# Kernel tuning notes

Measured on AMD Instinct MI355X. Metric: run time of the kernel, lower is better.

The kernel has to match this reference:

```python
import jax, jax.numpy as jnp
import numpy as np


def _pairwise_sqdist(x, y):
    # x: [B,N,D], y: [B,M,D] -> P: [B,N,M] squared euclidean distances
    xx = jnp.sum(x * x, axis=-1)            # [B,N]
    yy = jnp.sum(y * y, axis=-1)            # [B,M]
    zz = jnp.einsum('bnd,bmd->bnm', x, y)   # [B,N,M]
    return xx[:, :, None] + yy[:, None, :] - 2.0 * zz


def setup_inputs() -> dict:
    key = jax.random.key(0)
    k1, k2 = jax.random.split(key)
    B, N, M, D = 8, 4096, 4096, 256
    gts = jax.random.normal(k1, (B, N, D), dtype=jnp.float32)
    preds = jax.random.normal(k2, (B, M, D), dtype=jnp.float32)
    return {"gts": gts, "preds": preds}


def reference(gts, preds):
    P = _pairwise_sqdist(gts, preds)        # [B,N,M]
    loss_1 = jnp.sum(jnp.min(P, axis=1))    # min over gts dim (axis=1)
    loss_2 = jnp.sum(jnp.min(P, axis=2))    # min over preds dim (axis=2)
    return loss_1 + loss_2
```

## Files before the change

kernel.cpp:

```cpp
#include <hip/hip_runtime.h>

typedef int   i32x8 __attribute__((ext_vector_type(8)));
typedef float f32x4 __attribute__((ext_vector_type(4)));

#define B_   8
#define N_   4096
#define D_   256


__device__ __forceinline__ void gl_lds16(const void* g, void* l) {
  __builtin_amdgcn_global_load_lds(
      (const __attribute__((address_space(1))) unsigned int*)g,
      (__attribute__((address_space(3))) unsigned int*)l, 16, 0, 0);
}

__device__ __forceinline__ float sq8(unsigned w) {
  float f0 = __builtin_amdgcn_cvt_f32_fp8(w, 0);
  float f1 = __builtin_amdgcn_cvt_f32_fp8(w, 1);
  float f2 = __builtin_amdgcn_cvt_f32_fp8(w, 2);
  float f3 = __builtin_amdgcn_cvt_f32_fp8(w, 3);
  return f0 * f0 + f1 * f1 + f2 * f2 + f3 * f3;
}

__global__ __launch_bounds__(256) void prep_kernel(
    const float* __restrict__ x, const float* __restrict__ y,
    unsigned char* __restrict__ Xf, unsigned char* __restrict__ Yf,
    float* __restrict__ xx, float* __restrict__ yy,
    unsigned* __restrict__ rowmin, unsigned* __restrict__ colmin,
    float* __restrict__ out)
{
  __shared__ unsigned char T[4][16 * 272];
  if (blockIdx.x == 0 && threadIdx.x == 0) out[0] = 0.f;

  const int wv = threadIdx.x >> 6, lane = threadIdx.x & 63;
  const int wid = (blockIdx.x << 2) + wv;

  const float* src; unsigned char* dst; float* nrm; unsigned* mn; int g;
  if (wid < 2048) { g = wid;        src = x; dst = Xf; nrm = xx; mn = rowmin; }
  else            { g = wid - 2048; src = y; dst = Yf; nrm = yy; mn = colmin; }

  unsigned char* tw = T[wv];
  const float* rp = src + (size_t)g * 16 * D_;
#pragma unroll
  for (int r = 0; r < 16; ++r) {
    float4 v = *(const float4*)(rp + r * D_ + lane * 4);
    unsigned u = __builtin_amdgcn_cvt_pk_fp8_f32(v.x, v.y, 0, 0);
    u = __builtin_amdgcn_cvt_pk_fp8_f32(v.z, v.w, u, 1);
    *(unsigned*)(tw + r * 272 + lane * 4) = u;
  }
  asm volatile("s_waitcnt lgkmcnt(0)" ::: "memory");
  __builtin_amdgcn_wave_barrier();

  float s = 0.f;
  const int row = lane & 15, ko = (lane >> 4) * 32;
#pragma unroll
  for (int kt = 0; kt < 2; ++kt)
#pragma unroll
    for (int h = 0; h < 2; ++h) {
      uint4 c = *(const uint4*)(tw + row * 272 + kt * 128 + ko + h * 16);
      s += sq8(c.x) + sq8(c.y) + sq8(c.z) + sq8(c.w);
      *(uint4*)(dst + ((((size_t)g * 2 + kt) * 2 + h) << 10) + lane * 16) = c;
    }
  s += __shfl_xor(s, 16, 64);
  s += __shfl_xor(s, 32, 64);
  if      (lane < 16) nrm[g * 16 + lane] = s;
  else if (lane < 32) mn[g * 16 + lane - 16] = 0x7f800000u;
}

__global__ __launch_bounds__(256, 4) void chamfer_gemm(
    const unsigned char* __restrict__ Xf, const unsigned char* __restrict__ Yf,
    const float* __restrict__ xx, const float* __restrict__ yy,
    unsigned* __restrict__ rowmin, unsigned* __restrict__ colmin)
{
  __shared__ __align__(16) unsigned char S[4][8192];
  __shared__ unsigned cmin_s[1024];

  const int bid = blockIdx.x;
  const int b   = bid & 7;
  const int rt  = (bid >> 3) & 31;
  const int cq  = bid >> 8;
  const int n0  = rt * 128;
  const int m0  = cq * 1024;

  const int t = threadIdx.x, lane = t & 63, wave = t >> 6;
  const int quad = lane >> 4, lcol = lane & 15;

#pragma unroll
  for (int i = 0; i < 4; ++i) cmin_s[t + i * 256] = 0x7f800000u;

  i32x8 af[2][2];
#pragma unroll
  for (int i = 0; i < 2; ++i) {
    const size_t g = (size_t)(b * 256 + rt * 8 + wave * 2 + i);
#pragma unroll
    for (int kt = 0; kt < 2; ++kt) {
      const uint4* p = (const uint4*)(Xf + ((g * 2 + kt) << 11));
      uint4* h = (uint4*)&af[i][kt];
      h[0] = p[lane];
      h[1] = p[64 + lane];
    }
  }

  float xv[2][4], rmin[2][4];
  const float* xxp = xx + b * N_ + n0 + wave * 32;
#pragma unroll
  for (int i = 0; i < 2; ++i)
#pragma unroll
    for (int r = 0; r < 4; ++r) {
      xv[i][r] = xxp[i * 16 + quad * 4 + r];
      rmin[i][r] = 1e30f;
    }

  const unsigned char* Ybase = Yf + ((size_t)(b * 256 + cq * 64) << 12);
  const float* yyp = yy + b * N_ + m0;

#define STAGE_B(ct_, buf_)                                                    \
  {                                                                           \
    const unsigned char* Ysrc = Ybase + ((size_t)(ct_) << 13);     \
    _Pragma("unroll")                                                         \
    for (int h2 = 0; h2 < 2; ++h2) {                                          \
      int s  = t + h2 * 256;                                                  \
      int cd = s >> 6, ln = s & 63;                                           \
      int kt = cd >> 2, hh = (cd >> 1) & 1, jj = cd & 1;                      \
      gl_lds16(Ysrc + jj * 4096 + kt * 2048 + hh * 1024 + ln * 16,            \
               (buf_) + s * 16);                                              \
    }                                                                         \
  }

  auto do_ct = [&](int ct, const unsigned char* curb) {
    float yv0 = yyp[ct * 32 + lcol];
    float yv1 = yyp[ct * 32 + 16 + lcol];

    i32x8 bq[2][2];
#pragma unroll
    for (int j = 0; j < 2; ++j)
#pragma unroll
      for (int kt = 0; kt < 2; ++kt) {
        uint4* h = (uint4*)&bq[j][kt];
        h[0] = *(const uint4*)(curb + (kt * 4 + 0 + j) * 1024 + lane * 16);
        h[1] = *(const uint4*)(curb + (kt * 4 + 2 + j) * 1024 + lane * 16);
      }

    f32x4 acc[2][2] = {};
    __builtin_amdgcn_s_setprio(1);
#pragma unroll
    for (int kt = 0; kt < 2; ++kt)
#pragma unroll
      for (int i = 0; i < 2; ++i)
#pragma unroll
        for (int j = 0; j < 2; ++j)
          acc[i][j] = __builtin_amdgcn_mfma_scale_f32_16x16x128_f8f6f4(
              af[i][kt], bq[j][kt], acc[i][j],
              0, 0,
              0, 127,
              0, 127);
    __builtin_amdgcn_s_setprio(0);

#pragma unroll
    for (int j = 0; j < 2; ++j) {
      float yv = j ? yv1 : yv0;
      float cm = 1e30f;
#pragma unroll
      for (int i = 0; i < 2; ++i)
#pragma unroll
        for (int r = 0; r < 4; ++r) {
          float a = acc[i][j][r];
          rmin[i][r] = fminf(rmin[i][r], __builtin_fmaf(-2.0f, a, yv));
          cm         = fminf(cm,         __builtin_fmaf(-2.0f, a, xv[i][r]));
        }
      atomicMin(&cmin_s[ct * 32 + j * 16 + lcol], __float_as_uint(cm + yv));
    }
  };

  STAGE_B(0, S[0]);
  STAGE_B(1, S[1]);

  for (int g = 0; g < 16; ++g) {
    __syncthreads();
    const int cur = (g & 1) * 2;
    if (g + 1 < 16) {
      const int nxt = ((g + 1) & 1) * 2;
      STAGE_B(2 * g + 2, S[nxt]);
      STAGE_B(2 * g + 3, S[nxt + 1]);
    }
    do_ct(2 * g,     S[cur]);
    do_ct(2 * g + 1, S[cur + 1]);
  }

#pragma unroll
  for (int i = 0; i < 2; ++i)
#pragma unroll
    for (int r = 0; r < 4; ++r) {
      float v = xv[i][r] + rmin[i][r];
#pragma unroll
      for (int m = 1; m < 16; m <<= 1) v = fminf(v, __shfl_xor(v, m, 64));
      if (lcol == 0)
        atomicMin(rowmin + b * N_ + n0 + wave * 32 + i * 16 + quad * 4 + r,
                  __float_as_uint(v));
    }

  __syncthreads();
#pragma unroll
  for (int i = 0; i < 4; ++i) {
    int idx = t + i * 256;
    atomicMin(colmin + b * N_ + m0 + idx, cmin_s[idx]);
  }
#undef STAGE_B
}

__global__ __launch_bounds__(256) void reduce_kernel(
    const unsigned* __restrict__ mins,
    float* __restrict__ out)
{
  int idx = blockIdx.x * 256 + threadIdx.x;
  uint4 u = ((const uint4*)mins)[idx];
  float s = __uint_as_float(u.x) + __uint_as_float(u.y)
          + __uint_as_float(u.z) + __uint_as_float(u.w);
#pragma unroll
  for (int m = 1; m < 64; m <<= 1) s += __shfl_xor(s, m, 64);
  if ((threadIdx.x & 63) == 0) atomicAdd(out, s);
}

extern "C" void kernel_launch(void* const* d_in, const int* in_sizes, int n_in,
                              void* d_out, int out_size, void* d_ws, size_t ws_size,
                              hipStream_t stream) {
  const float* gts   = (const float*)d_in[0];
  const float* preds = (const float*)d_in[1];

  char* ws = (char*)d_ws;
  const size_t XB_BYTES = (size_t)B_ * N_ * D_;
  unsigned char* Xf     = (unsigned char*)ws;
  unsigned char* Yf     = (unsigned char*)(ws + XB_BYTES);
  float*    xx     = (float*)(ws + 2 * XB_BYTES);
  float*    yy     = (float*)(ws + 2 * XB_BYTES + (size_t)B_ * N_ * 4);
  unsigned* rowmin = (unsigned*)(ws + 2 * XB_BYTES + (size_t)B_ * N_ * 8);
  unsigned* colmin = (unsigned*)(ws + 2 * XB_BYTES + (size_t)B_ * N_ * 12);

  prep_kernel<<<1024, 256, 0, stream>>>(gts, preds, Xf, Yf, xx, yy, rowmin, colmin,
                                        (float*)d_out);

  chamfer_gemm<<<1024, 256, 0, stream>>>(Xf, Yf, xx, yy, rowmin, colmin);

  reduce_kernel<<<64, 256, 0, stream>>>(rowmin, (float*)d_out);
}
```

Measured before the change: 135.5 us.

## Halve per-block column span, double grid and target 8 blocks per CU

Each chamfer_gemm block now covers 512 prediction columns instead of 1024, so the grid doubles to 2048 blocks. Per-block LDS shrinks and each column tile is 16 wide instead of 32, with the B staging reduced to one 16-byte load per thread. Launch bounds ask for 8 blocks per CU to raise occupancy and improve load balance. In exchange, each block reuses its A fragments over less work, makes more global colmin atomics, and has less MFMA work per staged tile to hide latency. The in-kernel loop still runs 16 iterations of two column tiles, which matches the halved span.

```diff
diff --git a/kernel.cpp b/kernel.cpp
--- a/kernel.cpp
+++ b/kernel.cpp
@@ -67,26 +67,26 @@
   else if (lane < 32) mn[g * 16 + lane - 16] = 0x7f800000u;
 }
 
-__global__ __launch_bounds__(256, 4) void chamfer_gemm(
+__global__ __launch_bounds__(256, 8) void chamfer_gemm(
     const unsigned char* __restrict__ Xf, const unsigned char* __restrict__ Yf,
     const float* __restrict__ xx, const float* __restrict__ yy,
     unsigned* __restrict__ rowmin, unsigned* __restrict__ colmin)
 {
-  __shared__ __align__(16) unsigned char S[4][8192];
-  __shared__ unsigned cmin_s[1024];
+  __shared__ __align__(16) unsigned char S[4][4096];
+  __shared__ unsigned cmin_s[512];
 
   const int bid = blockIdx.x;
   const int b   = bid & 7;
   const int rt  = (bid >> 3) & 31;
   const int cq  = bid >> 8;
   const int n0  = rt * 128;
-  const int m0  = cq * 1024;
+  const int m0  = cq * 512;
 
   const int t = threadIdx.x, lane = t & 63, wave = t >> 6;
   const int quad = lane >> 4, lcol = lane & 15;
 
-#pragma unroll
-  for (int i = 0; i < 4; ++i) cmin_s[t + i * 256] = 0x7f800000u;
+  cmin_s[t]       = 0x7f800000u;
+  cmin_s[t + 256] = 0x7f800000u;
 
   i32x8 af[2][2];
 #pragma unroll
@@ -111,65 +111,46 @@
       rmin[i][r] = 1e30f;
     }
 
-  const unsigned char* Ybase = Yf + ((size_t)(b * 256 + cq * 64) << 12);
+  const unsigned char* Ybase = Yf + ((size_t)(b * 256 + cq * 32) << 12);
   const float* yyp = yy + b * N_ + m0;
 
 #define STAGE_B(ct_, buf_)                                                    \
-  {                                                                           \
-    const unsigned char* Ysrc = Ybase + ((size_t)(ct_) << 13);     \
-    _Pragma("unroll")                                                         \
-    for (int h2 = 0; h2 < 2; ++h2) {                                          \
-      int s  = t + h2 * 256;                                                  \
-      int cd = s >> 6, ln = s & 63;                                           \
-      int kt = cd >> 2, hh = (cd >> 1) & 1, jj = cd & 1;                      \
-      gl_lds16(Ysrc + jj * 4096 + kt * 2048 + hh * 1024 + ln * 16,            \
-               (buf_) + s * 16);                                              \
-    }                                                                         \
-  }
+  gl_lds16(Ybase + (((size_t)(ct_)) << 12) + t * 16, (buf_) + t * 16);
 
   auto do_ct = [&](int ct, const unsigned char* curb) {
-    float yv0 = yyp[ct * 32 + lcol];
-    float yv1 = yyp[ct * 32 + 16 + lcol];
-
-    i32x8 bq[2][2];
-#pragma unroll
-    for (int j = 0; j < 2; ++j)
-#pragma unroll
-      for (int kt = 0; kt < 2; ++kt) {
-        uint4* h = (uint4*)&bq[j][kt];
-        h[0] = *(const uint4*)(curb + (kt * 4 + 0 + j) * 1024 + lane * 16);
-        h[1] = *(const uint4*)(curb + (kt * 4 + 2 + j) * 1024 + lane * 16);
+    float yv = yyp[ct * 16 + lcol];
+
+    f32x4 acc[2] = {};
+#pragma unroll
+    for (int kt = 0; kt < 2; ++kt) {
+      i32x8 bq;
+      uint4* h = (uint4*)&bq;
+      h[0] = *(const uint4*)(curb + kt * 2048 + lane * 16);
+      h[1] = *(const uint4*)(curb + kt * 2048 + 1024 + lane * 16);
+      __builtin_amdgcn_s_setprio(1);
+#pragma unroll
+      for (int i = 0; i < 2; ++i)
+        acc[i] = __builtin_amdgcn_mfma_scale_f32_16x16x128_f8f6f4(
+            af[i][kt], bq, acc[i],
+            0, 0,
+            0, 127,
+            0, 127);
+      __builtin_amdgcn_s_setprio(0);
+    }
+
+    float tc[8];
+#pragma unroll
+    for (int i = 0; i < 2; ++i)
+#pragma unroll
+      for (int r = 0; r < 4; ++r) {
+        float a = acc[i][r];
+        rmin[i][r] = fminf(rmin[i][r], __builtin_fmaf(-2.0f, a, yv));
+        tc[i * 4 + r] = __builtin_fmaf(-2.0f, a, xv[i][r]);
       }
-
-    f32x4 acc[2][2] = {};
-    __builtin_amdgcn_s_setprio(1);
-#pragma unroll
-    for (int kt = 0; kt < 2; ++kt)
-#pragma unroll
-      for (int i = 0; i < 2; ++i)
-#pragma unroll
-        for (int j = 0; j < 2; ++j)
-          acc[i][j] = __builtin_amdgcn_mfma_scale_f32_16x16x128_f8f6f4(
-              af[i][kt], bq[j][kt], acc[i][j],
-              0, 0,
-              0, 127,
-              0, 127);
-    __builtin_amdgcn_s_setprio(0);
-
-#pragma unroll
-    for (int j = 0; j < 2; ++j) {
-      float yv = j ? yv1 : yv0;
-      float cm = 1e30f;
-#pragma unroll
-      for (int i = 0; i < 2; ++i)
-#pragma unroll
-        for (int r = 0; r < 4; ++r) {
-          float a = acc[i][j][r];
-          rmin[i][r] = fminf(rmin[i][r], __builtin_fmaf(-2.0f, a, yv));
-          cm         = fminf(cm,         __builtin_fmaf(-2.0f, a, xv[i][r]));
-        }
-      atomicMin(&cmin_s[ct * 32 + j * 16 + lcol], __float_as_uint(cm + yv));
-    }
+    float m1 = fminf(fminf(tc[0], tc[1]), tc[2]);
+    float m2 = fminf(fminf(tc[3], tc[4]), tc[5]);
+    float cm = fminf(fminf(m1, m2), fminf(tc[6], tc[7]));
+    atomicMin(&cmin_s[ct * 16 + lcol], __float_as_uint(cm + yv));
   };
 
   STAGE_B(0, S[0]);
@@ -201,7 +182,7 @@
 
   __syncthreads();
 #pragma unroll
-  for (int i = 0; i < 4; ++i) {
+  for (int i = 0; i < 2; ++i) {
     int idx = t + i * 256;
     atomicMin(colmin + b * N_ + m0 + idx, cmin_s[idx]);
   }
@@ -239,7 +220,7 @@
   prep_kernel<<<1024, 256, 0, stream>>>(gts, preds, Xf, Yf, xx, yy, rowmin, colmin,
                                         (float*)d_out);
 
-  chamfer_gemm<<<1024, 256, 0, stream>>>(Xf, Yf, xx, yy, rowmin, colmin);
+  chamfer_gemm<<<2048, 256, 0, stream>>>(Xf, Yf, xx, yy, rowmin, colmin);
 
   reduce_kernel<<<64, 256, 0, stream>>>(rowmin, (float*)d_out);
 }
```

Result: slower. 373.7 us (+175.9%).
